# Kernel tuning notes

Hardware: AMD Instinct MI355X
Metric: run time of the kernel (lower is better)

The kernel has to match this reference:

```python
import jax, jax.numpy as jnp
import numpy as np

B, S_SRC, S_TGT = 32, 64, 1024
D, H, DFF, LE, LD, V = 128, 8, 512, 6, 6, 64


def _pe(S, d):
    # PyTorch-style sinusoidal positional encoding, shape [S, d]
    pos = np.arange(S, dtype=np.float32)[:, None]
    div = np.exp(np.arange(0, d, 2, dtype=np.float32) * (-np.log(10000.0) / d))
    pe = np.zeros((S, d), dtype=np.float32)
    pe[:, 0::2] = np.sin(pos * div)
    pe[:, 1::2] = np.cos(pos * div)
    return jnp.asarray(pe)


def _ln(x, g, b, eps=1e-5):
    m = x.mean(-1, keepdims=True)
    v = ((x - m) ** 2).mean(-1, keepdims=True)
    return (x - m) / jnp.sqrt(v + eps) * g + b


def _mha(q_in, k_in, v_in, Wqkv, bqkv, Wo, bo):
    d = q_in.shape[-1]
    dh = d // H
    def proj(x, W, b):
        return (x @ W.T + b).reshape(x.shape[0], x.shape[1], H, dh)
    q = proj(q_in, Wqkv[:d], bqkv[:d])
    k = proj(k_in, Wqkv[d:2 * d], bqkv[d:2 * d])
    v = proj(v_in, Wqkv[2 * d:], bqkv[2 * d:])
    scores = jnp.einsum('bqhd,bkhd->bhqk', q, k) * (1.0 / np.sqrt(dh))
    a = jax.nn.softmax(scores, axis=-1)
    o = jnp.einsum('bhqk,bkhd->bqhd', a, v).reshape(q_in.shape[0], q_in.shape[1], d)
    return o @ Wo.T + bo


def _ffn(x, W1, b1, W2, b2):
    return jax.nn.relu(x @ W1.T + b1) @ W2.T + b2


def reference(src, tgt, emb,
              enc_qkv_w, enc_qkv_b, enc_out_w, enc_out_b,
              enc_ln1_g, enc_ln1_b, enc_ff1_w, enc_ff1_b,
              enc_ff2_w, enc_ff2_b, enc_ln2_g, enc_ln2_b,
              enc_norm_g, enc_norm_b,
              dec_sa_qkv_w, dec_sa_qkv_b, dec_sa_out_w, dec_sa_out_b,
              dec_ln1_g, dec_ln1_b,
              dec_ca_qkv_w, dec_ca_qkv_b, dec_ca_out_w, dec_ca_out_b,
              dec_ln2_g, dec_ln2_b,
              dec_ff1_w, dec_ff1_b, dec_ff2_w, dec_ff2_b,
              dec_ln3_g, dec_ln3_b, dec_norm_g, dec_norm_b,
              fc_w, fc_b):
    # src: [B, S_SRC] int tokens (occupation config); tgt: [B, S_TGT, D] (zeros in the original)
    s = emb[src] * np.sqrt(float(D)) + _pe(src.shape[1], D)
    t = tgt + _pe(tgt.shape[1], D)
    # encoder (post-norm, ReLU, dropout=0 in eval)
    for i in range(LE):
        s = _ln(s + _mha(s, s, s, enc_qkv_w[i], enc_qkv_b[i], enc_out_w[i], enc_out_b[i]),
                enc_ln1_g[i], enc_ln1_b[i])
        s = _ln(s + _ffn(s, enc_ff1_w[i], enc_ff1_b[i], enc_ff2_w[i], enc_ff2_b[i]),
                enc_ln2_g[i], enc_ln2_b[i])
    mem = _ln(s, enc_norm_g, enc_norm_b)
    # decoder
    for i in range(LD):
        t = _ln(t + _mha(t, t, t, dec_sa_qkv_w[i], dec_sa_qkv_b[i], dec_sa_out_w[i], dec_sa_out_b[i]),
                dec_ln1_g[i], dec_ln1_b[i])
        t = _ln(t + _mha(t, mem, mem, dec_ca_qkv_w[i], dec_ca_qkv_b[i], dec_ca_out_w[i], dec_ca_out_b[i]),
                dec_ln2_g[i], dec_ln2_b[i])
        t = _ln(t + _ffn(t, dec_ff1_w[i], dec_ff1_b[i], dec_ff2_w[i], dec_ff2_b[i]),
                dec_ln3_g[i], dec_ln3_b[i])
    t = _ln(t, dec_norm_g, dec_norm_b)
    return t @ fc_w.T + fc_b  # [B, S_TGT, 1] transformer correction to TN params


def setup_inputs():
    ks = iter(jax.random.split(jax.random.key(0), 64))
    def nrm(shape, scale=0.02):
        return jax.random.normal(next(ks), shape, dtype=jnp.float32) * scale
    inp = {
        'src': jax.random.randint(next(ks), (B, S_SRC), 0, V),
        'tgt': jnp.zeros((B, S_TGT, D), jnp.float32),
        'emb': nrm((V, D), 1.0),
        'enc_qkv_w': nrm((LE, 3 * D, D)), 'enc_qkv_b': jnp.zeros((LE, 3 * D)),
        'enc_out_w': nrm((LE, D, D)), 'enc_out_b': jnp.zeros((LE, D)),
        'enc_ln1_g': jnp.ones((LE, D)), 'enc_ln1_b': jnp.zeros((LE, D)),
        'enc_ff1_w': nrm((LE, DFF, D)), 'enc_ff1_b': jnp.zeros((LE, DFF)),
        'enc_ff2_w': nrm((LE, D, DFF)), 'enc_ff2_b': jnp.zeros((LE, D)),
        'enc_ln2_g': jnp.ones((LE, D)), 'enc_ln2_b': jnp.zeros((LE, D)),
        'enc_norm_g': jnp.ones((D,)), 'enc_norm_b': jnp.zeros((D,)),
        'dec_sa_qkv_w': nrm((LD, 3 * D, D)), 'dec_sa_qkv_b': jnp.zeros((LD, 3 * D)),
        'dec_sa_out_w': nrm((LD, D, D)), 'dec_sa_out_b': jnp.zeros((LD, D)),
        'dec_ln1_g': jnp.ones((LD, D)), 'dec_ln1_b': jnp.zeros((LD, D)),
        'dec_ca_qkv_w': nrm((LD, 3 * D, D)), 'dec_ca_qkv_b': jnp.zeros((LD, 3 * D)),
        'dec_ca_out_w': nrm((LD, D, D)), 'dec_ca_out_b': jnp.zeros((LD, D)),
        'dec_ln2_g': jnp.ones((LD, D)), 'dec_ln2_b': jnp.zeros((LD, D)),
        'dec_ff1_w': nrm((LD, DFF, D)), 'dec_ff1_b': jnp.zeros((LD, DFF)),
        'dec_ff2_w': nrm((LD, D, DFF)), 'dec_ff2_b': jnp.zeros((LD, D)),
        'dec_ln3_g': jnp.ones((LD, D)), 'dec_ln3_b': jnp.zeros((LD, D)),
        'dec_norm_g': jnp.ones((D,)), 'dec_norm_b': jnp.zeros((D,)),
        'fc_w': nrm((1, D)), 'fc_b': jnp.zeros((1,)),
    }
    return inp
```

## Files before the change

kernel.cpp:

```cpp
#include <hip/hip_runtime.h>
#include <hip/hip_bf16.h>
#include <stdint.h>

#define NH 8

typedef uint16_t u16;
typedef __attribute__((ext_vector_type(8))) short s8b;
typedef __attribute__((ext_vector_type(4))) float f32x4;
typedef __attribute__((ext_vector_type(16))) float f32x16;

__device__ __forceinline__ u16 f2b(float f) {
    uint32_t u = __builtin_bit_cast(uint32_t, f);
    u = (u + 0x7fffu + ((u >> 16) & 1u)) >> 16;
    return (u16)u;
}

__device__ __forceinline__ float pe_val(int pos, int d) {
    int j = d >> 1;
    float div = expf((float)j * -0.14391156831212787f);
    float ang = (float)pos * div;
    return (d & 1) ? cosf(ang) : sinf(ang);
}

__global__ void embed_kernel(const int* __restrict__ src, const float* __restrict__ emb,
                             float* __restrict__ S, u16* __restrict__ Sb) {
    int idx = blockIdx.x * 256 + threadIdx.x;
    int d = idx & 127;
    int n = idx >> 7;
    int i = n & 63;
    int tok = src[n];
    float v = emb[tok * 128 + d] * 11.313708498984761f + pe_val(i, d);
    S[idx] = v; Sb[idx] = f2b(v);
}

__global__ void addpe_kernel(const float* __restrict__ tgt, float* __restrict__ T,
                             u16* __restrict__ Tb) {
    int idx = blockIdx.x * 256 + threadIdx.x;
    int d = idx & 127;
    int n = idx >> 7;
    int i = n & 1023;
    float v = tgt[idx] + pe_val(i, d);
    T[idx] = v; Tb[idx] = f2b(v);
}

struct CvtJobs { const float* src[10]; u16* dst[10]; int n[10]; };
__global__ void cvt_kernel(CvtJobs jb) {
    int e = blockIdx.y;
    int i = blockIdx.x * 256 + threadIdx.x;
    if (i < jb.n[e]) jb.dst[e][i] = f2b(jb.src[e][i]);
}

__global__ void transposeV(const u16* __restrict__ KV, int stride, int voff,
                           u16* __restrict__ VT, int SKV) {
    int bh = blockIdx.x;
    int k0 = blockIdx.y * 64;
    int l = threadIdx.x;
    int b = bh >> 3, h = bh & 7;
    const u16* p = KV + (size_t)(b * SKV + k0 + l) * stride + voff + h * 16;
    s8b v0 = *(const s8b*)p;
    s8b v1 = *(const s8b*)(p + 8);
    size_t obase = (size_t)bh * 16 * SKV + k0 + l;
#pragma unroll
    for (int n = 0; n < 8; n++) VT[obase + (size_t)n * SKV] = (u16)v0[n];
#pragma unroll
    for (int n = 0; n < 8; n++) VT[obase + (size_t)(n + 8) * SKV] = (u16)v1[n];
}

template <int RELU>
__global__ __launch_bounds__(256) void gemm_mfma(const u16* __restrict__ A,
                                                 const u16* __restrict__ W,
                                                 const float* __restrict__ bias,
                                                 u16* __restrict__ C,
                                                 int M, int N, int K) {
    __shared__ __align__(16) u16 As[128 * 56];
    __shared__ __align__(16) u16 Bs[128 * 56];
    int tid = threadIdx.x;
    int lane = tid & 63, w = tid >> 6;
    int quad = lane >> 4, l15 = lane & 15;
    int m0 = blockIdx.y * 128, n0 = blockIdx.x * 128;
    int wm = (w & 1) * 64, wn = (w >> 1) * 64;
    int srow = tid >> 1, skof = (tid & 1) * 16;

    f32x4 acc[4][4];
#pragma unroll
    for (int i = 0; i < 4; i++)
#pragma unroll
        for (int j = 0; j < 4; j++)
#pragma unroll
            for (int r = 0; r < 4; r++) acc[i][j][r] = 0.f;

    for (int k0 = 0; k0 < K; k0 += 32) {
        const u16* ga = A + (size_t)(m0 + srow) * K + k0 + skof;
        const u16* gw = W + (size_t)(n0 + srow) * K + k0 + skof;
        s8b a0 = *(const s8b*)ga, a1 = *(const s8b*)(ga + 8);
        s8b w0 = *(const s8b*)gw, w1 = *(const s8b*)(gw + 8);
        __syncthreads();
        *(s8b*)(As + srow * 56 + skof) = a0;
        *(s8b*)(As + srow * 56 + skof + 8) = a1;
        *(s8b*)(Bs + srow * 56 + skof) = w0;
        *(s8b*)(Bs + srow * 56 + skof + 8) = w1;
        __syncthreads();
        s8b af[4], bfr[4];
#pragma unroll
        for (int i = 0; i < 4; i++) af[i] = *(const s8b*)(As + (wm + 16 * i + l15) * 56 + quad * 8);
#pragma unroll
        for (int j = 0; j < 4; j++) bfr[j] = *(const s8b*)(Bs + (wn + 16 * j + l15) * 56 + quad * 8);
#pragma unroll
        for (int i = 0; i < 4; i++)
#pragma unroll
            for (int j = 0; j < 4; j++)
                acc[i][j] = __builtin_amdgcn_mfma_f32_16x16x32_bf16(af[i], bfr[j], acc[i][j], 0, 0, 0);
    }
#pragma unroll
    for (int j = 0; j < 4; j++) {
        int col = n0 + wn + 16 * j + l15;
        float bv = bias[col];
#pragma unroll
        for (int i = 0; i < 4; i++) {
            int rbase = m0 + wm + 16 * i + quad * 4;
#pragma unroll
            for (int r = 0; r < 4; r++) {
                float v = acc[i][j][r] + bv;
                if (RELU) v = fmaxf(v, 0.f);
                C[(size_t)(rbase + r) * N + col] = f2b(v);
            }
        }
    }
}

__global__ __launch_bounds__(256) void gemm_ln(const u16* __restrict__ A,
                                               const u16* __restrict__ W,
                                               const float* __restrict__ bias,
                                               const float* __restrict__ X,
                                               const float* __restrict__ g,
                                               const float* __restrict__ bta,
                                               float* __restrict__ Y,
                                               u16* __restrict__ Yb,
                                               int M, int K) {
    __shared__ __align__(16) u16 As[128 * 56];
    __shared__ __align__(16) u16 Bs[128 * 56];
    __shared__ float redS[128][2], redQ[128][2];
    int tid = threadIdx.x;
    int lane = tid & 63, w = tid >> 6;
    int quad = lane >> 4, l15 = lane & 15;
    int m0 = blockIdx.x * 128;
    int wm = (w & 1) * 64, wn = (w >> 1) * 64;
    int srow = tid >> 1, skof = (tid & 1) * 16;

    f32x4 acc[4][4];
#pragma unroll
    for (int i = 0; i < 4; i++)
#pragma unroll
        for (int j = 0; j < 4; j++)
#pragma unroll
            for (int r = 0; r < 4; r++) acc[i][j][r] = 0.f;

    for (int k0 = 0; k0 < K; k0 += 32) {
        const u16* ga = A + (size_t)(m0 + srow) * K + k0 + skof;
        const u16* gw = W + (size_t)srow * K + k0 + skof;
        s8b a0 = *(const s8b*)ga, a1 = *(const s8b*)(ga + 8);
        s8b w0 = *(const s8b*)gw, w1 = *(const s8b*)(gw + 8);
        __syncthreads();
        *(s8b*)(As + srow * 56 + skof) = a0;
        *(s8b*)(As + srow * 56 + skof + 8) = a1;
        *(s8b*)(Bs + srow * 56 + skof) = w0;
        *(s8b*)(Bs + srow * 56 + skof + 8) = w1;
        __syncthreads();
        s8b af[4], bfr[4];
#pragma unroll
        for (int i = 0; i < 4; i++) af[i] = *(const s8b*)(As + (wm + 16 * i + l15) * 56 + quad * 8);
#pragma unroll
        for (int j = 0; j < 4; j++) bfr[j] = *(const s8b*)(Bs + (wn + 16 * j + l15) * 56 + quad * 8);
#pragma unroll
        for (int i = 0; i < 4; i++)
#pragma unroll
            for (int j = 0; j < 4; j++)
                acc[i][j] = __builtin_amdgcn_mfma_f32_16x16x32_bf16(af[i], bfr[j], acc[i][j], 0, 0, 0);
    }

    float s_[4][4], q_[4][4];
#pragma unroll
    for (int i = 0; i < 4; i++)
#pragma unroll
        for (int r = 0; r < 4; r++) {
            int row = m0 + wm + 16 * i + quad * 4 + r;
            float s = 0.f, q = 0.f;
#pragma unroll
            for (int j = 0; j < 4; j++) {
                int col = wn + 16 * j + l15;
                float x = acc[i][j][r] + bias[col] + X[(size_t)row * 128 + col];
                acc[i][j][r] = x;
                s += x; q += x * x;
            }
#pragma unroll
            for (int off = 1; off < 16; off <<= 1) {
                s += __shfl_xor(s, off);
                q += __shfl_xor(q, off);
            }
            s_[i][r] = s; q_[i][r] = q;
        }
    if (l15 == 0) {
#pragma unroll
        for (int i = 0; i < 4; i++)
#pragma unroll
            for (int r = 0; r < 4; r++) {
                int lrow = wm + 16 * i + quad * 4 + r;
                redS[lrow][wn >> 6] = s_[i][r];
                redQ[lrow][wn >> 6] = q_[i][r];
            }
    }
    __syncthreads();
#pragma unroll
    for (int i = 0; i < 4; i++)
#pragma unroll
        for (int r = 0; r < 4; r++) {
            int lrow = wm + 16 * i + quad * 4 + r;
            int row = m0 + lrow;
            float S2 = redS[lrow][0] + redS[lrow][1];
            float Q2 = redQ[lrow][0] + redQ[lrow][1];
            float mean = S2 * (1.f / 128.f);
            float var = Q2 * (1.f / 128.f) - mean * mean;
            float rstd = rsqrtf(var + 1e-5f);
#pragma unroll
            for (int j = 0; j < 4; j++) {
                int col = wn + 16 * j + l15;
                float y = (acc[i][j][r] - mean) * rstd * g[col] + bta[col];
                Y[(size_t)row * 128 + col] = y;
                Yb[(size_t)row * 128 + col] = f2b(y);
            }
        }
}

template <int WAVES>
__global__ __launch_bounds__(WAVES * 64) void attn2(
    const u16* __restrict__ Qb, int qstride, int qoff,
    const u16* __restrict__ Kb, int kstride, int koff,
    const u16* __restrict__ VT,
    u16* __restrict__ O, int SQ, int SKV) {
    __shared__ __align__(16) u16 Ps[WAVES][32 * 56];
    int tid = threadIdx.x;
    int lane = tid & 63, w = tid >> 6;
    int quad = lane >> 4, l15 = lane & 15, l31 = lane & 31, half = lane >> 5;
    int nqc = SQ / (WAVES * 32);
    int bid = blockIdx.x;
    int qc = bid % nqc;
    int h = (bid / nqc) % NH;
    int b = bid / (nqc * NH);
    int q0 = qc * WAVES * 32 + w * 32;

    const u16* qp = Qb + (size_t)(b * SQ + q0 + l31) * qstride + qoff + h * 16 + half * 8;
    s8b qf = *(const s8b*)qp;
    s8b ones;
#pragma unroll
    for (int j = 0; j < 8; j++) ones[j] = (short)0x3F80;

    const u16* vtb = VT + ((size_t)(b * NH + h) * 16 + l15) * SKV + quad * 8;
    const u16* kp = Kb + (size_t)(b * SKV + l31) * kstride + koff + h * 16 + half * 8;
    size_t kadv = (size_t)32 * kstride;

    f32x4 O0, O1, L0, L1;
#pragma unroll
    for (int r = 0; r < 4; r++) { O0[r] = 0.f; O1[r] = 0.f; L0[r] = 0.f; L1[r] = 0.f; }

    u16* pw = Ps[w];
    for (int j0 = 0; j0 < SKV; j0 += 32) {
        s8b kf = *(const s8b*)kp;
        kp += kadv;
        s8b vb = *(const s8b*)(vtb + j0);
        f32x16 S;
#pragma unroll
        for (int r = 0; r < 16; r++) S[r] = 0.f;
        S = __builtin_amdgcn_mfma_f32_32x32x16_bf16(qf, kf, S, 0, 0, 0);
#pragma unroll
        for (int r = 0; r < 16; r++) {
            float p = __expf(S[r] * 0.25f);
            int row = (r & 3) + 8 * (r >> 2) + 4 * half;
            pw[row * 56 + l31] = f2b(p);
        }
        __builtin_amdgcn_wave_barrier();
        s8b pa0 = *(const s8b*)(pw + l15 * 56 + quad * 8);
        s8b pa1 = *(const s8b*)(pw + (16 + l15) * 56 + quad * 8);
        O0 = __builtin_amdgcn_mfma_f32_16x16x32_bf16(pa0, vb, O0, 0, 0, 0);
        O1 = __builtin_amdgcn_mfma_f32_16x16x32_bf16(pa1, vb, O1, 0, 0, 0);
        L0 = __builtin_amdgcn_mfma_f32_16x16x32_bf16(pa0, ones, L0, 0, 0, 0);
        L1 = __builtin_amdgcn_mfma_f32_16x16x32_bf16(pa1, ones, L1, 0, 0, 0);
    }
#pragma unroll
    for (int r = 0; r < 4; r++) {
        int q = b * SQ + q0 + quad * 4 + r;
        O[(size_t)q * 128 + h * 16 + l15] = f2b(O0[r] / L0[r]);
        O[(size_t)(q + 16) * 128 + h * 16 + l15] = f2b(O1[r] / L1[r]);
    }
}

__global__ void ln_kernel(const float* __restrict__ X, const float* __restrict__ R,
                          const float* __restrict__ g, const float* __restrict__ bta,
                          float* __restrict__ Y, u16* __restrict__ Yb) {
    int r = blockIdx.x;
    int lane = threadIdx.x;
    size_t base = (size_t)r * 128;
    float x0 = X[base + lane], x1 = X[base + lane + 64];
    if (R) { x0 += R[base + lane]; x1 += R[base + lane + 64]; }
    float s = x0 + x1;
    for (int off = 32; off; off >>= 1) s += __shfl_xor(s, off);
    float mean = s * (1.f / 128.f);
    float d0 = x0 - mean, d1 = x1 - mean;
    float vs = d0 * d0 + d1 * d1;
    for (int off = 32; off; off >>= 1) vs += __shfl_xor(vs, off);
    float rstd = rsqrtf(vs * (1.f / 128.f) + 1e-5f);
    float y0 = d0 * rstd * g[lane] + bta[lane];
    float y1 = d1 * rstd * g[lane + 64] + bta[lane + 64];
    Y[base + lane] = y0;
    Y[base + lane + 64] = y1;
    if (Yb) { Yb[base + lane] = f2b(y0); Yb[base + lane + 64] = f2b(y1); }
}

__global__ void fc_kernel(const float* __restrict__ X, const float* __restrict__ w,
                          const float* __restrict__ b, float* __restrict__ out) {
    int r = blockIdx.x;
    int lane = threadIdx.x;
    size_t base = (size_t)r * 128;
    float s = X[base + lane] * w[lane] + X[base + lane + 64] * w[lane + 64];
    for (int off = 32; off; off >>= 1) s += __shfl_xor(s, off);
    if (lane == 0) out[r] = s + b[0];
}

static inline void gemm_b(const u16* A, const u16* W, const float* bias, u16* C,
                          int M, int N, int K, hipStream_t st) {
    hipLaunchKernelGGL((gemm_mfma<0>), dim3(N / 128, M / 128), dim3(256), 0, st,
                       A, W, bias, C, M, N, K);
}
static inline void gemm_br(const u16* A, const u16* W, const float* bias, u16* C,
                           int M, int N, int K, hipStream_t st) {
    hipLaunchKernelGGL((gemm_mfma<1>), dim3(N / 128, M / 128), dim3(256), 0, st,
                       A, W, bias, C, M, N, K);
}
static inline void gemmln(const u16* A, const u16* W, const float* bias,
                          const float* X, const float* g, const float* bta,
                          float* Y, u16* Yb, int M, int K, hipStream_t st) {
    hipLaunchKernelGGL(gemm_ln, dim3(M / 128), dim3(256), 0, st,
                       A, W, bias, X, g, bta, Y, Yb, M, K);
}

extern "C" void kernel_launch(void* const* d_in, const int* in_sizes, int n_in,
                              void* d_out, int out_size, void* d_ws, size_t ws_size,
                              hipStream_t stream) {
    const int B = 32, SSRC = 64, STGT = 1024, D = 128, DFF_ = 512, LE = 6, LD = 6;

    const int*   src = (const int*)d_in[0];
    const float* tgt = (const float*)d_in[1];
    const float* emb = (const float*)d_in[2];
    const float* enc_qkv_w = (const float*)d_in[3];
    const float* enc_qkv_b = (const float*)d_in[4];
    const float* enc_out_w = (const float*)d_in[5];
    const float* enc_out_b = (const float*)d_in[6];
    const float* enc_ln1_g = (const float*)d_in[7];
    const float* enc_ln1_b = (const float*)d_in[8];
    const float* enc_ff1_w = (const float*)d_in[9];
    const float* enc_ff1_b = (const float*)d_in[10];
    const float* enc_ff2_w = (const float*)d_in[11];
    const float* enc_ff2_b = (const float*)d_in[12];
    const float* enc_ln2_g = (const float*)d_in[13];
    const float* enc_ln2_b = (const float*)d_in[14];
    const float* enc_norm_g = (const float*)d_in[15];
    const float* enc_norm_b = (const float*)d_in[16];
    const float* dec_sa_qkv_w = (const float*)d_in[17];
    const float* dec_sa_qkv_b = (const float*)d_in[18];
    const float* dec_sa_out_w = (const float*)d_in[19];
    const float* dec_sa_out_b = (const float*)d_in[20];
    const float* dec_ln1_g = (const float*)d_in[21];
    const float* dec_ln1_b = (const float*)d_in[22];
    const float* dec_ca_qkv_w = (const float*)d_in[23];
    const float* dec_ca_qkv_b = (const float*)d_in[24];
    const float* dec_ca_out_w = (const float*)d_in[25];
    const float* dec_ca_out_b = (const float*)d_in[26];
    const float* dec_ln2_g = (const float*)d_in[27];
    const float* dec_ln2_b = (const float*)d_in[28];
    const float* dec_ff1_w = (const float*)d_in[29];
    const float* dec_ff1_b = (const float*)d_in[30];
    const float* dec_ff2_w = (const float*)d_in[31];
    const float* dec_ff2_b = (const float*)d_in[32];
    const float* dec_ln3_g = (const float*)d_in[33];
    const float* dec_ln3_b = (const float*)d_in[34];
    const float* dec_norm_g = (const float*)d_in[35];
    const float* dec_norm_b = (const float*)d_in[36];
    const float* fc_w = (const float*)d_in[37];
    const float* fc_b = (const float*)d_in[38];

    const int NT = B * STGT;
    const int NS = B * SSRC;

    float* t_f   = (float*)d_ws;
    float* s_f   = t_f + (size_t)NT * D;
    float* mem_f = s_f + (size_t)NS * D;
    u16* t_bf    = (u16*)(mem_f + (size_t)NS * D);
    u16* s_bf    = t_bf + (size_t)NT * D;
    u16* mem_bf  = s_bf + (size_t)NS * D;
    u16* qkv_bf  = mem_bf + (size_t)NS * D;
    u16* attno_bf = qkv_bf + (size_t)NT * DFF_;
    u16* ckv_bf  = attno_bf + (size_t)NT * D;
    u16* vt      = ckv_bf + (size_t)NS * 2 * D;
    u16* wa      = vt + (size_t)B * NH * 16 * STGT;

    u16* w_enc_qkv = wa;                          int n_enc_qkv = LE * 3 * D * D;
    u16* w_enc_out = w_enc_qkv + n_enc_qkv;       int n_enc_out = LE * D * D;
    u16* w_enc_ff1 = w_enc_out + n_enc_out;       int n_enc_ff1 = LE * DFF_ * D;
    u16* w_enc_ff2 = w_enc_ff1 + n_enc_ff1;       int n_enc_ff2 = LE * D * DFF_;
    u16* w_sa_qkv  = w_enc_ff2 + n_enc_ff2;       int n_sa_qkv = LD * 3 * D * D;
    u16* w_sa_out  = w_sa_qkv + n_sa_qkv;         int n_sa_out = LD * D * D;
    u16* w_ca_qkv  = w_sa_out + n_sa_out;         int n_ca_qkv = LD * 3 * D * D;
    u16* w_ca_out  = w_ca_qkv + n_ca_qkv;         int n_ca_out = LD * D * D;
    u16* w_ff1     = w_ca_out + n_ca_out;         int n_ff1 = LD * DFF_ * D;
    u16* w_ff2     = w_ff1 + n_ff1;               int n_ff2 = LD * D * DFF_;

    float* scf = (float*)qkv_bf;

    CvtJobs jb;
    jb.src[0] = enc_qkv_w;    jb.dst[0] = w_enc_qkv; jb.n[0] = n_enc_qkv;
    jb.src[1] = enc_out_w;    jb.dst[1] = w_enc_out; jb.n[1] = n_enc_out;
    jb.src[2] = enc_ff1_w;    jb.dst[2] = w_enc_ff1; jb.n[2] = n_enc_ff1;
    jb.src[3] = enc_ff2_w;    jb.dst[3] = w_enc_ff2; jb.n[3] = n_enc_ff2;
    jb.src[4] = dec_sa_qkv_w; jb.dst[4] = w_sa_qkv;  jb.n[4] = n_sa_qkv;
    jb.src[5] = dec_sa_out_w; jb.dst[5] = w_sa_out;  jb.n[5] = n_sa_out;
    jb.src[6] = dec_ca_qkv_w; jb.dst[6] = w_ca_qkv;  jb.n[6] = n_ca_qkv;
    jb.src[7] = dec_ca_out_w; jb.dst[7] = w_ca_out;  jb.n[7] = n_ca_out;
    jb.src[8] = dec_ff1_w;    jb.dst[8] = w_ff1;     jb.n[8] = n_ff1;
    jb.src[9] = dec_ff2_w;    jb.dst[9] = w_ff2;     jb.n[9] = n_ff2;
    int maxn = n_enc_ff1;
    hipLaunchKernelGGL(cvt_kernel, dim3((maxn + 255) / 256, 10), dim3(256), 0, stream, jb);

    hipLaunchKernelGGL(embed_kernel, dim3(NS * D / 256), dim3(256), 0, stream, src, emb, s_f, s_bf);

    for (int i = 0; i < LE; i++) {
        gemm_b(s_bf, w_enc_qkv + (size_t)i * 3 * D * D, enc_qkv_b + (size_t)i * 3 * D,
               qkv_bf, NS, 3 * D, D, stream);
        hipLaunchKernelGGL(transposeV, dim3(B * NH, 1), dim3(64), 0, stream,
                           qkv_bf, 3 * D, 2 * D, vt, SSRC);
        hipLaunchKernelGGL((attn2<2>), dim3(B * NH), dim3(128), 0, stream,
                           qkv_bf, 3 * D, 0, qkv_bf, 3 * D, D, vt, attno_bf, SSRC, SSRC);
        gemmln(attno_bf, w_enc_out + (size_t)i * D * D, enc_out_b + (size_t)i * D,
               s_f, enc_ln1_g + (size_t)i * D, enc_ln1_b + (size_t)i * D, s_f, s_bf, NS, D, stream);
        gemm_br(s_bf, w_enc_ff1 + (size_t)i * DFF_ * D, enc_ff1_b + (size_t)i * DFF_,
                qkv_bf, NS, DFF_, D, stream);
        gemmln(qkv_bf, w_enc_ff2 + (size_t)i * D * DFF_, enc_ff2_b + (size_t)i * D,
               s_f, enc_ln2_g + (size_t)i * D, enc_ln2_b + (size_t)i * D, s_f, s_bf, NS, DFF_, stream);
    }
    hipLaunchKernelGGL(ln_kernel, dim3(NS), dim3(64), 0, stream,
                       s_f, (const float*)nullptr, enc_norm_g, enc_norm_b, mem_f, mem_bf);

    hipLaunchKernelGGL(addpe_kernel, dim3(NT * D / 256), dim3(256), 0, stream, tgt, t_f, t_bf);

    for (int i = 0; i < LD; i++) {
        gemm_b(t_bf, w_sa_qkv + (size_t)i * 3 * D * D, dec_sa_qkv_b + (size_t)i * 3 * D,
               qkv_bf, NT, 3 * D, D, stream);
        hipLaunchKernelGGL(transposeV, dim3(B * NH, STGT / 64), dim3(64), 0, stream,
                           qkv_bf, 3 * D, 2 * D, vt, STGT);
        hipLaunchKernelGGL((attn2<4>), dim3(B * NH * (STGT / 128)), dim3(256), 0, stream,
                           qkv_bf, 3 * D, 0, qkv_bf, 3 * D, D, vt, attno_bf, STGT, STGT);
        gemmln(attno_bf, w_sa_out + (size_t)i * D * D, dec_sa_out_b + (size_t)i * D,
               t_f, dec_ln1_g + (size_t)i * D, dec_ln1_b + (size_t)i * D, t_f, t_bf, NT, D, stream);

        gemm_b(t_bf, w_ca_qkv + (size_t)i * 3 * D * D, dec_ca_qkv_b + (size_t)i * 3 * D,
               qkv_bf, NT, D, D, stream);
        gemm_b(mem_bf, w_ca_qkv + (size_t)i * 3 * D * D + (size_t)D * D,
               dec_ca_qkv_b + (size_t)i * 3 * D + D, ckv_bf, NS, 2 * D, D, stream);
        hipLaunchKernelGGL(transposeV, dim3(B * NH, 1), dim3(64), 0, stream,
                           ckv_bf, 2 * D, D, vt, SSRC);
        hipLaunchKernelGGL((attn2<4>), dim3(B * NH * (STGT / 128)), dim3(256), 0, stream,
                           qkv_bf, D, 0, ckv_bf, 2 * D, 0, vt, attno_bf, STGT, SSRC);
        gemmln(attno_bf, w_ca_out + (size_t)i * D * D, dec_ca_out_b + (size_t)i * D,
               t_f, dec_ln2_g + (size_t)i * D, dec_ln2_b + (size_t)i * D, t_f, t_bf, NT, D, stream);

        gemm_br(t_bf, w_ff1 + (size_t)i * DFF_ * D, dec_ff1_b + (size_t)i * DFF_,
                qkv_bf, NT, DFF_, D, stream);
        gemmln(qkv_bf, w_ff2 + (size_t)i * D * DFF_, dec_ff2_b + (size_t)i * D,
               t_f, dec_ln3_g + (size_t)i * D, dec_ln3_b + (size_t)i * D, t_f, t_bf, NT, DFF_, stream);
    }

    hipLaunchKernelGGL(ln_kernel, dim3(NT), dim3(64), 0, stream,
                       t_f, (const float*)nullptr, dec_norm_g, dec_norm_b, scf, (u16*)nullptr);
    hipLaunchKernelGGL(fc_kernel, dim3(NT), dim3(64), 0, stream,
                       scf, fc_w, fc_b, (float*)d_out);
}
```

Measured before the change: 1.563 ms.

## Fold softmax scale into Q projection, use exp2 and packed bf16 P stores

The Q-projection GEMM epilogue now multiplies the Q columns by the attention scale times log2(e), so attention can call the hardware exp2 builtin directly without a per-score multiply. The score MFMA swaps operands to produce a transposed S tile, which lets each lane pack two bf16 probabilities into one 32-bit word with a perm instruction and write to a narrower LDS buffer. Fewer LDS store instructions and ALU ops are needed per tile, and the loop is unrolled by two. Rounding in the packed conversion changes from round-to-nearest-even to round-half-up, and Q is now stored already scaled in bf16, which slightly changes numerics.

```diff
diff --git a/kernel.cpp b/kernel.cpp
--- a/kernel.cpp
+++ b/kernel.cpp
@@ -5,14 +5,29 @@
 #define NH 8
 
 typedef uint16_t u16;
+typedef uint32_t u32;
 typedef __attribute__((ext_vector_type(8))) short s8b;
 typedef __attribute__((ext_vector_type(4))) float f32x4;
 typedef __attribute__((ext_vector_type(16))) float f32x16;
 
+#if __has_builtin(__builtin_amdgcn_exp2f)
+#define EXPS(x) __builtin_amdgcn_exp2f(x)
+#define QSCALE 0.36067376022224085f
+#else
+#define EXPS(x) __expf(x)
+#define QSCALE 0.25f
+#endif
+
 __device__ __forceinline__ u16 f2b(float f) {
-    uint32_t u = __builtin_bit_cast(uint32_t, f);
+    u32 u = __builtin_bit_cast(u32, f);
     u = (u + 0x7fffu + ((u >> 16) & 1u)) >> 16;
     return (u16)u;
+}
+
+__device__ __forceinline__ u32 pkbf(float a, float b) {
+    u32 ua = __builtin_bit_cast(u32, a) + 0x8000u;
+    u32 ub = __builtin_bit_cast(u32, b) + 0x8000u;
+    return __builtin_amdgcn_perm(ub, ua, 0x07060302);
 }
 
 __device__ __forceinline__ float pe_val(int pos, int d) {
@@ -71,7 +86,8 @@
                                                  const u16* __restrict__ W,
                                                  const float* __restrict__ bias,
                                                  u16* __restrict__ C,
-                                                 int M, int N, int K) {
+                                                 int M, int N, int K,
+                                                 float qscale, int qcols) {
     __shared__ __align__(16) u16 As[128 * 56];
     __shared__ __align__(16) u16 Bs[128 * 56];
     int tid = threadIdx.x;
@@ -115,12 +131,13 @@
     for (int j = 0; j < 4; j++) {
         int col = n0 + wn + 16 * j + l15;
         float bv = bias[col];
+        float sc = (col < qcols) ? qscale : 1.f;
 #pragma unroll
         for (int i = 0; i < 4; i++) {
             int rbase = m0 + wm + 16 * i + quad * 4;
 #pragma unroll
             for (int r = 0; r < 4; r++) {
-                float v = acc[i][j][r] + bv;
+                float v = (acc[i][j][r] + bv) * sc;
                 if (RELU) v = fmaxf(v, 0.f);
                 C[(size_t)(rbase + r) * N + col] = f2b(v);
             }
@@ -232,12 +249,12 @@
 }
 
 template <int WAVES>
-__global__ __launch_bounds__(WAVES * 64) void attn2(
+__global__ __launch_bounds__(WAVES * 64) void attn3(
     const u16* __restrict__ Qb, int qstride, int qoff,
     const u16* __restrict__ Kb, int kstride, int koff,
     const u16* __restrict__ VT,
     u16* __restrict__ O, int SQ, int SKV) {
-    __shared__ __align__(16) u16 Ps[WAVES][32 * 56];
+    __shared__ __align__(16) u32 Ps[WAVES][32 * 20];
     int tid = threadIdx.x;
     int lane = tid & 63, w = tid >> 6;
     int quad = lane >> 4, l15 = lane & 15, l31 = lane & 31, half = lane >> 5;
@@ -262,7 +279,8 @@
 #pragma unroll
     for (int r = 0; r < 4; r++) { O0[r] = 0.f; O1[r] = 0.f; L0[r] = 0.f; L1[r] = 0.f; }
 
-    u16* pw = Ps[w];
+    u32* pw = Ps[w];
+#pragma unroll 2
     for (int j0 = 0; j0 < SKV; j0 += 32) {
         s8b kf = *(const s8b*)kp;
         kp += kadv;
@@ -270,16 +288,20 @@
         f32x16 S;
 #pragma unroll
         for (int r = 0; r < 16; r++) S[r] = 0.f;
-        S = __builtin_amdgcn_mfma_f32_32x32x16_bf16(qf, kf, S, 0, 0, 0);
-#pragma unroll
-        for (int r = 0; r < 16; r++) {
-            float p = __expf(S[r] * 0.25f);
-            int row = (r & 3) + 8 * (r >> 2) + 4 * half;
-            pw[row * 56 + l31] = f2b(p);
+        S = __builtin_amdgcn_mfma_f32_32x32x16_bf16(kf, qf, S, 0, 0, 0);
+#pragma unroll
+        for (int g = 0; g < 4; g++) {
+            float p0 = EXPS(S[4 * g + 0]);
+            float p1 = EXPS(S[4 * g + 1]);
+            float p2 = EXPS(S[4 * g + 2]);
+            float p3 = EXPS(S[4 * g + 3]);
+            int kw = l31 * 20 + 2 * half + 4 * g;
+            pw[kw] = pkbf(p0, p1);
+            pw[kw + 1] = pkbf(p2, p3);
         }
         __builtin_amdgcn_wave_barrier();
-        s8b pa0 = *(const s8b*)(pw + l15 * 56 + quad * 8);
-        s8b pa1 = *(const s8b*)(pw + (16 + l15) * 56 + quad * 8);
+        s8b pa0 = *(const s8b*)(pw + l15 * 20 + quad * 4);
+        s8b pa1 = *(const s8b*)(pw + (16 + l15) * 20 + quad * 4);
         O0 = __builtin_amdgcn_mfma_f32_16x16x32_bf16(pa0, vb, O0, 0, 0, 0);
         O1 = __builtin_amdgcn_mfma_f32_16x16x32_bf16(pa1, vb, O1, 0, 0, 0);
         L0 = __builtin_amdgcn_mfma_f32_16x16x32_bf16(pa0, ones, L0, 0, 0, 0);
@@ -326,14 +348,14 @@
 }
 
 static inline void gemm_b(const u16* A, const u16* W, const float* bias, u16* C,
-                          int M, int N, int K, hipStream_t st) {
+                          int M, int N, int K, hipStream_t st, int qcols = 0) {
     hipLaunchKernelGGL((gemm_mfma<0>), dim3(N / 128, M / 128), dim3(256), 0, st,
-                       A, W, bias, C, M, N, K);
+                       A, W, bias, C, M, N, K, QSCALE, qcols);
 }
 static inline void gemm_br(const u16* A, const u16* W, const float* bias, u16* C,
                            int M, int N, int K, hipStream_t st) {
     hipLaunchKernelGGL((gemm_mfma<1>), dim3(N / 128, M / 128), dim3(256), 0, st,
-                       A, W, bias, C, M, N, K);
+                       A, W, bias, C, M, N, K, 1.f, 0);
 }
 static inline void gemmln(const u16* A, const u16* W, const float* bias,
                           const float* X, const float* g, const float* bta,
@@ -433,10 +455,10 @@
 
     for (int i = 0; i < LE; i++) {
         gemm_b(s_bf, w_enc_qkv + (size_t)i * 3 * D * D, enc_qkv_b + (size_t)i * 3 * D,
-               qkv_bf, NS, 3 * D, D, stream);
+               qkv_bf, NS, 3 * D, D, stream, 128);
         hipLaunchKernelGGL(transposeV, dim3(B * NH, 1), dim3(64), 0, stream,
                            qkv_bf, 3 * D, 2 * D, vt, SSRC);
-        hipLaunchKernelGGL((attn2<2>), dim3(B * NH), dim3(128), 0, stream,
+        hipLaunchKernelGGL((attn3<2>), dim3(B * NH), dim3(128), 0, stream,
                            qkv_bf, 3 * D, 0, qkv_bf, 3 * D, D, vt, attno_bf, SSRC, SSRC);
         gemmln(attno_bf, w_enc_out + (size_t)i * D * D, enc_out_b + (size_t)i * D,
                s_f, enc_ln1_g + (size_t)i * D, enc_ln1_b + (size_t)i * D, s_f, s_bf, NS, D, stream);
@@ -452,21 +474,21 @@
 
     for (int i = 0; i < LD; i++) {
         gemm_b(t_bf, w_sa_qkv + (size_t)i * 3 * D * D, dec_sa_qkv_b + (size_t)i * 3 * D,
-               qkv_bf, NT, 3 * D, D, stream);
+               qkv_bf, NT, 3 * D, D, stream, 128);
         hipLaunchKernelGGL(transposeV, dim3(B * NH, STGT / 64), dim3(64), 0, stream,
                            qkv_bf, 3 * D, 2 * D, vt, STGT);
-        hipLaunchKernelGGL((attn2<4>), dim3(B * NH * (STGT / 128)), dim3(256), 0, stream,
+        hipLaunchKernelGGL((attn3<4>), dim3(B * NH * (STGT / 128)), dim3(256), 0, stream,
                            qkv_bf, 3 * D, 0, qkv_bf, 3 * D, D, vt, attno_bf, STGT, STGT);
         gemmln(attno_bf, w_sa_out + (size_t)i * D * D, dec_sa_out_b + (size_t)i * D,
                t_f, dec_ln1_g + (size_t)i * D, dec_ln1_b + (size_t)i * D, t_f, t_bf, NT, D, stream);
 
         gemm_b(t_bf, w_ca_qkv + (size_t)i * 3 * D * D, dec_ca_qkv_b + (size_t)i * 3 * D,
-               qkv_bf, NT, D, D, stream);
+               qkv_bf, NT, D, D, stream, 128);
         gemm_b(mem_bf, w_ca_qkv + (size_t)i * 3 * D * D + (size_t)D * D,
                dec_ca_qkv_b + (size_t)i * 3 * D + D, ckv_bf, NS, 2 * D, D, stream);
         hipLaunchKernelGGL(transposeV, dim3(B * NH, 1), dim3(64), 0, stream,
                            ckv_bf, 2 * D, D, vt, SSRC);
-        hipLaunchKernelGGL((attn2<4>), dim3(B * NH * (STGT / 128)), dim3(256), 0, stream,
+        hipLaunchKernelGGL((attn3<4>), dim3(B * NH * (STGT / 128)), dim3(256), 0, stream,
                            qkv_bf, D, 0, ckv_bf, 2 * D, 0, vt, attno_bf, STGT, SSRC);
         gemmln(attno_bf, w_ca_out + (size_t)i * D * D, dec_ca_out_b + (size_t)i * D,
                t_f, dec_ln2_g + (size_t)i * D, dec_ln2_b + (size_t)i * D, t_f, t_bf, NT, D, stream);
```

After: 1.508 ms. 3.5% less time.
